# Kernel optimization log

Hardware: AMD Instinct MI355X
Metric: run time of the kernel (lower is better)

## Reference

```python
import jax, jax.numpy as jnp
import numpy as np

B = 2048; IN_DIM = 60; TTL = 30; H = 512; L = 5; OUT = 23
T_PTS = 90; SUB = 10  # fixed-step RK4 substeps per day (stands in for per-sample dopri5)
P_D = 0.2; P_H = 0.15; P_V = 0.25  # DELPHI fixed detection/hospitalization/ventilation fractions
LN2 = float(np.log(2.0))
R_I = LN2/5.0; R_D = LN2/2.0; R_RI = LN2/10.0; R_RH = LN2/15.0; R_RV = LN2/10.0


def setup_inputs():
    ks = jax.random.split(jax.random.key(0), 24)
    w = lambda k, s: (jax.random.normal(k, s) * 0.05).astype(jnp.float32)
    rng = jnp.array([1.0]*11 + [1.0, 60.0, 4.0, 0.5, 0.3, 0.5, 5.0, 5.0, 2.0, 60.0, 30.0, 1.0], dtype=jnp.float32)
    return {
        'model_input': jax.random.normal(ks[0], (B, IN_DIM), dtype=jnp.float32),
        'population': jax.random.uniform(ks[1], (B,), minval=1e5, maxval=1e7, dtype=jnp.float32),
        'cumulative_case_number': jax.random.uniform(ks[2], (B, 1), minval=1e3, maxval=1e5, dtype=jnp.float32),
        'mortality_rate': jax.random.uniform(ks[3], (B,), minval=0.01, maxval=0.05, dtype=jnp.float32),
        'h0': jax.random.normal(ks[4], (L, B, H), dtype=jnp.float32),
        'c0': jax.random.normal(ks[5], (L, B, H), dtype=jnp.float32),
        'W_ih0': w(ks[6], (4*H, TTL)),
        'W_ihR': w(ks[7], (L-1, 4*H, H)),
        'W_hh': w(ks[8], (L, 4*H, H)),
        'b_ih': w(ks[9], (L, 4*H)),
        'b_hh': w(ks[10], (L, 4*H)),
        'meta_W1': w(ks[11], (H, IN_DIM - TTL)), 'meta_b1': w(ks[12], (H,)),
        'meta_W2': w(ks[13], (H, H)), 'meta_b2': w(ks[14], (H,)),
        'ro_W1': w(ks[15], (2*H, 2*H)), 'ro_b1': w(ks[16], (2*H,)),
        'ro_W2': w(ks[17], (OUT, 2*H)), 'ro_b2': w(ks[18], (OUT,)),
        'dnn_output_range': rng,
        'sigmoid_scale': 1,
    }


def _backbone(model_input, population, h0, c0, W_ih0, W_ihR, W_hh, b_ih, b_hh,
              meta_W1, meta_b1, meta_W2, meta_b2, ro_W1, ro_b1, ro_W2, ro_b2,
              dnn_output_range, sigmoid_scale):
    x = model_input[:, :TTL] / population[:, None]
    for l in range(L):  # single-timestep, 5-layer LSTM; torch gate order i,f,g,o
        Wi = W_ih0 if l == 0 else W_ihR[l-1]
        g = x @ Wi.T + b_ih[l] + h0[l] @ W_hh[l].T + b_hh[l]
        gi, gf, gg, go = jnp.split(g, 4, axis=1)
        c = jax.nn.sigmoid(gf) * c0[l] + jax.nn.sigmoid(gi) * jnp.tanh(gg)
        x = jax.nn.sigmoid(go) * jnp.tanh(c)
    ts_out = x  # [B, H]
    m = jax.nn.relu(model_input[:, TTL:] @ meta_W1.T + meta_b1)
    m = jax.nn.relu(m @ meta_W2.T + meta_b2)
    z = jnp.concatenate([ts_out, m], axis=1)  # [B, 2H]
    z = jnp.tanh(z @ ro_W1.T + ro_b1)
    raw = z @ ro_W2.T + ro_b2  # [B, OUT]
    dnn = jax.nn.sigmoid(raw * sigmoid_scale) * dnn_output_range
    return dnn, ts_out, raw


def _ode(dnn, population, cumulative_case_number, mortality_rate):
    p = dnn[:, 11:]  # 12 fitted DELPHI params per sample
    alpha, days, r_s, r_dth, p_dth, r_dthdecay, k1, k2, jump, t_jump, std_normal, k3 = [p[:, j] for j in range(12)]
    N = population
    PopI = cumulative_case_number[:, 0]
    PopD = jnp.floor(mortality_rate * PopI)
    R_0 = jnp.where(PopI - PopD > 5.0 * PopD, 5.0 * PopD, 0.0)
    PopCI = PopI - PopD - R_0
    # DELPHI initial conditions
    S0 = N - (PopCI/P_D)*(k1 + k2) - R_0/P_D - PopD/P_D
    y0 = jnp.stack([
        S0,
        PopCI/P_D*k1,                      # E
        PopCI/P_D*k2,                      # I
        (PopCI/P_D - PopCI)*(1.0 - p_dth), # AR
        PopCI*P_H*(1.0 - p_dth),           # DHR
        PopCI*(1.0 - P_H)*(1.0 - p_dth),   # DQR
        (PopCI/P_D - PopCI)*p_dth,         # AD
        PopCI*P_H*p_dth,                   # DHD
        PopCI*(1.0 - P_H)*p_dth,           # DQD
        R_0/P_D,                           # R
        PopD/P_D,                          # D
        PopCI*P_H,                         # TH
        PopCI*P_H*P_V*(1.0 - p_dth),       # DVR
        PopCI*P_H*P_V*p_dth,               # DVD
        PopD,                              # DD
        PopI,                              # DT
    ], axis=1)  # [B, 16]

    def deriv(t, y):
        S, E, I = y[:, 0], y[:, 1], y[:, 2]
        AR, DHR, DQR, AD, DHD, DQD = y[:, 3], y[:, 4], y[:, 5], y[:, 6], y[:, 7], y[:, 8]
        DVR, DVD = y[:, 12], y[:, 13]
        gam = (2.0/jnp.pi)*jnp.arctan(-(t - days)/20.0*r_s) + 1.0 \
              + jump*jnp.exp(-(t - t_jump)**2/(2.0*std_normal**2))
        pdt = (2.0/jnp.pi)*(p_dth - 0.001)*(jnp.arctan(-t*r_dthdecay/20.0) + jnp.pi/2.0) + 0.001
        inf = alpha*gam*S*I/N
        det = R_D*I
        return jnp.stack([
            -inf,
            inf - R_I*E,
            R_I*E - det,
            det*(1.0-pdt)*(1.0-P_D) - R_RI*AR,
            det*(1.0-pdt)*P_D*P_H - R_RH*DHR,
            det*(1.0-pdt)*P_D*(1.0-P_H) - R_RI*DQR,
            det*pdt*(1.0-P_D) - r_dth*AD,
            det*pdt*P_D*P_H - r_dth*DHD,
            det*pdt*P_D*(1.0-P_H) - r_dth*DQD,
            R_RI*(AR + DQR) + R_RH*DHR,
            r_dth*(AD + DQD + DHD),
            det*P_D*P_H,
            det*(1.0-pdt)*P_D*P_H*P_V - R_RV*DVR,
            det*pdt*P_D*P_H*P_V - r_dth*DVD,
            r_dth*(DHD + DQD),
            det*P_D,
        ], axis=1)

    dt = 1.0 / SUB

    def segment(y, t0):
        def sub(yy, j):
            t = t0 + j*dt
            k1_ = deriv(t, yy)
            k2_ = deriv(t + 0.5*dt, yy + 0.5*dt*k1_)
            k3_ = deriv(t + 0.5*dt, yy + 0.5*dt*k2_)
            k4_ = deriv(t + dt, yy + dt*k3_)
            return yy + (dt/6.0)*(k1_ + 2.0*k2_ + 2.0*k3_ + k4_), None
        y2, _ = jax.lax.scan(sub, y, jnp.arange(SUB, dtype=jnp.float32))
        return y2, y2

    _, ys = jax.lax.scan(segment, y0, jnp.arange(T_PTS - 1, dtype=jnp.float32))
    sol = jnp.concatenate([y0[None], ys], axis=0)  # [T_PTS, B, 16]
    return jnp.transpose(sol, (1, 0, 2))  # [B, T_PTS, 16]


def reference(model_input, population, cumulative_case_number, mortality_rate, h0, c0,
              W_ih0, W_ihR, W_hh, b_ih, b_hh, meta_W1, meta_b1, meta_W2, meta_b2,
              ro_W1, ro_b1, ro_W2, ro_b2, dnn_output_range, sigmoid_scale):
    dnn, ts_out, raw = _backbone(model_input, population, h0, c0, W_ih0, W_ihR, W_hh,
                                 b_ih, b_hh, meta_W1, meta_b1, meta_W2, meta_b2,
                                 ro_W1, ro_b1, ro_W2, ro_b2, dnn_output_range, sigmoid_scale)
    sol = _ode(dnn, population, cumulative_case_number, mortality_rate)
    return sol, dnn, ts_out[:, None, :], raw
```

## Files before the change

kernel.cpp:

```cpp
#include <hip/hip_runtime.h>
#include <hip/hip_bf16.h>
#include <math.h>

#define BATCH 2048
#define HID 512
#define TPTS 90
#define NSEG 89
#define NSUB 10
#define NSTEPS 890

#if defined(__has_builtin)
#if __has_builtin(__builtin_amdgcn_global_load_lds)
#define HAS_GLL 1
#endif
#endif
#ifndef HAS_GLL
#define HAS_GLL 0
#endif

__device__ __constant__ const float kR_I  = 0.6931471805599453f / 5.0f;
__device__ __constant__ const float kR_D  = 0.6931471805599453f / 2.0f;
__device__ __constant__ const float kR_RI = 0.6931471805599453f / 10.0f;
__device__ __constant__ const float kR_RH = 0.6931471805599453f / 15.0f;
__device__ __constant__ const float kR_RV = 0.6931471805599453f / 10.0f;

typedef __attribute__((ext_vector_type(8))) short short8;
typedef __attribute__((ext_vector_type(4))) short short4v;
typedef __attribute__((ext_vector_type(4))) float float4v;

__device__ __forceinline__ float sigmoidf_(float x) { return 1.0f / (1.0f + expf(-x)); }

#if HAS_GLL
__device__ __forceinline__ void gll16(const void* g, void* l) {
    __builtin_amdgcn_global_load_lds(
        (const __attribute__((address_space(1))) unsigned int*)g,
        (__attribute__((address_space(3))) unsigned int*)l, 16, 0, 0);
}
#endif

__global__ void prep_pad(const float* __restrict__ mi, const float* __restrict__ pop,
                         const float* __restrict__ Wih0, const float* __restrict__ mW1,
                         float* __restrict__ x0p, float* __restrict__ xmp,
                         float* __restrict__ Wp0, float* __restrict__ Wpm)
{
    int i = blockIdx.x * 256 + threadIdx.x;
    int r = i >> 5, c = i & 31;
    bool v = (c < 30);
    x0p[i] = v ? mi[r * 60 + c] / pop[r] : 0.0f;
    xmp[i] = v ? mi[r * 60 + 30 + c] : 0.0f;
    Wp0[i] = v ? Wih0[r * 30 + c] : 0.0f;
    if (r < 512) Wpm[i] = v ? mW1[r * 30 + c] : 0.0f;
}

__device__ __forceinline__ void pack_quad(const float* __restrict__ s1, int ld1, int K1,
                                          const float* __restrict__ s2, int ld2, int K2,
                                          __hip_bfloat16* __restrict__ dst, int idx, bool wm)
{
    int Ks = K1 + K2, Kq = Ks >> 2;
    int r = idx / Kq, k4 = (idx - r * Kq) << 2;
    const float* srcp; int base, seg, kk;
    if (k4 < K1) { srcp = s1 + (size_t)r * ld1 + k4; base = 0; seg = K1; kk = k4; }
    else { kk = k4 - K1; srcp = s2 + (size_t)r * ld2 + kk; base = 3 * K1; seg = K2; }
    float4 x = *(const float4*)srcp;
    union { __hip_bfloat16 b[4]; short4v v; } H, L;
    H.b[0] = __float2bfloat16(x.x); H.b[1] = __float2bfloat16(x.y);
    H.b[2] = __float2bfloat16(x.z); H.b[3] = __float2bfloat16(x.w);
    L.b[0] = __float2bfloat16(x.x - __bfloat162float(H.b[0]));
    L.b[1] = __float2bfloat16(x.y - __bfloat162float(H.b[1]));
    L.b[2] = __float2bfloat16(x.z - __bfloat162float(H.b[2]));
    L.b[3] = __float2bfloat16(x.w - __bfloat162float(H.b[3]));
    __hip_bfloat16* d = dst + (size_t)r * (3 * Ks) + base;
    *(short4v*)(d + kk)           = H.v;
    *(short4v*)(d + seg + kk)     = wm ? L.v : H.v;
    *(short4v*)(d + 2 * seg + kk) = wm ? H.v : L.v;
}

__global__ void pack_pair(const float* __restrict__ a1, int alda1, int aK1,
                          const float* __restrict__ a2, int alda2, int aK2,
                          __hip_bfloat16* __restrict__ da, int arows,
                          const float* __restrict__ w1, int wld1, int wK1,
                          const float* __restrict__ w2, int wld2, int wK2,
                          __hip_bfloat16* __restrict__ dw, int wrows)
{
    int aKq = (aK1 + aK2) >> 2, wKq = (wK1 + wK2) >> 2;
    int qa = arows * aKq;
    int idx = blockIdx.x * 256 + threadIdx.x;
    if (idx < qa) {
        pack_quad(a1, alda1, aK1, a2, alda2, aK2, da, idx, false);
    } else {
        idx -= qa;
        if (idx < wrows * wKq) pack_quad(w1, wld1, wK1, w2, wld2, wK2, dw, idx, true);
    }
}

template<int ACT>
__global__ __launch_bounds__(256, 2)
void gemm_mfma(const __hip_bfloat16* __restrict__ Ah,
               const __hip_bfloat16* __restrict__ Wh, int K3,
               const float* __restrict__ b1, const float* __restrict__ b2,
               float* __restrict__ Cp, int ldc, int N)
{
    __shared__ __hip_bfloat16 As[128 * 32];
    __shared__ __hip_bfloat16 Ws[64 * 32];
    const int tid  = threadIdx.x;
    const int m0   = blockIdx.y * 128;
    const int n0   = blockIdx.x * 64;
    const int lane = tid & 63, wv = tid >> 6;
    const int mw   = (wv >> 1) * 64, nw = (wv & 1) * 32;
    const int l15  = lane & 15, quad = lane >> 4;
    const int sr   = tid >> 2;
    const int sc   = (tid & 3) * 8;

    float4v acc[4][2];
    #pragma unroll
    for (int i = 0; i < 4; ++i)
        #pragma unroll
        for (int j = 0; j < 2; ++j)
            acc[i][j] = (float4v){0.0f, 0.0f, 0.0f, 0.0f};

    const __hip_bfloat16* pa0 = Ah + (size_t)(m0 + sr)      * K3 + sc;
    const __hip_bfloat16* pa1 = Ah + (size_t)(m0 + sr + 64) * K3 + sc;
    const __hip_bfloat16* pw0 = Wh + (size_t)(n0 + sr)      * K3 + sc;

#if HAS_GLL
    char* ldsA0 = (char*)As + wv * 1024;
    char* ldsA1 = (char*)As + 4096 + wv * 1024;
    char* ldsW0 = (char*)Ws + wv * 1024;
#endif

#if !HAS_GLL
    short8 a0 = *(const short8*)(pa0);
    short8 a1 = *(const short8*)(pa1);
    short8 w0 = *(const short8*)(pw0);
#endif

    for (int kt = 0; kt < K3; kt += 32) {
#if HAS_GLL
        __syncthreads();
        gll16(pa0 + kt, ldsA0);
        gll16(pa1 + kt, ldsA1);
        gll16(pw0 + kt, ldsW0);
        __syncthreads();
#else
        __syncthreads();
        *(short8*)(As + sr * 32 + sc)        = a0;
        *(short8*)(As + (sr + 64) * 32 + sc) = a1;
        *(short8*)(Ws + sr * 32 + sc)        = w0;
        __syncthreads();
        int kn = kt + 32;
        if (kn < K3) {
            a0 = *(const short8*)(pa0 + kn);
            a1 = *(const short8*)(pa1 + kn);
            w0 = *(const short8*)(pw0 + kn);
        }
#endif
        short8 af[4], bf[2];
        #pragma unroll
        for (int t = 0; t < 4; ++t)
            af[t] = *(const short8*)(As + (mw + t * 16 + l15) * 32 + quad * 8);
        #pragma unroll
        for (int t = 0; t < 2; ++t)
            bf[t] = *(const short8*)(Ws + (nw + t * 16 + l15) * 32 + quad * 8);
        #pragma unroll
        for (int i = 0; i < 4; ++i)
            #pragma unroll
            for (int j = 0; j < 2; ++j)
                acc[i][j] = __builtin_amdgcn_mfma_f32_16x16x32_bf16(af[i], bf[j], acc[i][j], 0, 0, 0);
    }

    #pragma unroll
    for (int j = 0; j < 2; ++j) {
        int col = n0 + nw + j * 16 + l15;
        float bias = b1[col] + (b2 ? b2[col] : 0.0f);
        #pragma unroll
        for (int i = 0; i < 4; ++i) {
            #pragma unroll
            for (int r = 0; r < 4; ++r) {
                int row = m0 + mw + i * 16 + quad * 4 + r;
                float v = acc[i][j][r] + bias;
                if (ACT == 1)      v = fmaxf(v, 0.0f);
                else if (ACT == 2) v = tanhf(v);
                Cp[(size_t)row * ldc + col] = v;
            }
        }
    }
}

template<int ACT>
__global__ __launch_bounds__(256)
void gemm_dual(const float* __restrict__ A1, int lda1,
               const float* __restrict__ W1, int ldw1, int K1,
               const float* __restrict__ A2, int lda2,
               const float* __restrict__ W2, int ldw2, int K2,
               const float* __restrict__ b1p, const float* __restrict__ b2p,
               float* __restrict__ Cp, int ldc, int N)
{
    __shared__ float As[8][128];
    __shared__ float Ws[8][128];
    const int tid  = threadIdx.x;
    const int m0   = blockIdx.y * 128;
    const int n0   = blockIdx.x * 128;
    const int tm   = tid >> 4;
    const int tn   = tid & 15;
    const int lrow = tid >> 1;
    const int lkh  = (tid & 1) << 2;
    const int wrow = n0 + lrow;
    const int Ktot = K1 + K2;

    float acc[8][8];
    #pragma unroll
    for (int i = 0; i < 8; ++i)
        #pragma unroll
        for (int j = 0; j < 8; ++j) acc[i][j] = 0.0f;

    float4 av = *(const float4*)(A1 + (size_t)(m0 + lrow) * lda1 + lkh);
    float4 wv = make_float4(0.0f, 0.0f, 0.0f, 0.0f);
    if (wrow < N) wv = *(const float4*)(W1 + (size_t)wrow * ldw1 + lkh);

    for (int kt = 0; kt < Ktot; kt += 8) {
        __syncthreads();
        As[lkh + 0][lrow] = av.x; As[lkh + 1][lrow] = av.y;
        As[lkh + 2][lrow] = av.z; As[lkh + 3][lrow] = av.w;
        Ws[lkh + 0][lrow] = wv.x; Ws[lkh + 1][lrow] = wv.y;
        Ws[lkh + 2][lrow] = wv.z; Ws[lkh + 3][lrow] = wv.w;
        __syncthreads();

        int kn = kt + 8;
        float4 avn = make_float4(0.0f, 0.0f, 0.0f, 0.0f);
        float4 wvn = avn;
        if (kn < Ktot) {
            if (kn < K1) {
                avn = *(const float4*)(A1 + (size_t)(m0 + lrow) * lda1 + kn + lkh);
                if (wrow < N) wvn = *(const float4*)(W1 + (size_t)wrow * ldw1 + kn + lkh);
            } else {
                int k2 = kn - K1;
                avn = *(const float4*)(A2 + (size_t)(m0 + lrow) * lda2 + k2 + lkh);
                if (wrow < N) wvn = *(const float4*)(W2 + (size_t)wrow * ldw2 + k2 + lkh);
            }
        }

        #pragma unroll
        for (int kk = 0; kk < 8; ++kk) {
            float af[8], wf[8];
            #pragma unroll
            for (int i = 0; i < 4; ++i) {
                af[i]     = As[kk][tm * 8 + i];
                af[i + 4] = As[kk][tm * 8 + 4 + i];
                wf[i]     = Ws[kk][tn * 4 + i];
                wf[i + 4] = Ws[kk][64 + tn * 4 + i];
            }
            #pragma unroll
            for (int i = 0; i < 8; ++i)
                #pragma unroll
                for (int j = 0; j < 8; ++j)
                    acc[i][j] += af[i] * wf[j];
        }
        av = avn; wv = wvn;
    }

    #pragma unroll
    for (int j = 0; j < 8; ++j) {
        int col = n0 + ((j < 4) ? (tn * 4 + j) : (64 + tn * 4 + (j - 4)));
        if (col >= N) continue;
        float bias = b1p[col] + (b2p ? b2p[col] : 0.0f);
        #pragma unroll
        for (int i = 0; i < 8; ++i) {
            int rrow = m0 + tm * 8 + i;
            float v = acc[i][j] + bias;
            if (ACT == 1) v = fmaxf(v, 0.0f);
            else if (ACT == 2) v = tanhf(v);
            Cp[(size_t)rrow * ldc + col] = v;
        }
    }
}

__global__ __launch_bounds__(256)
void gemv_ro2(const float* __restrict__ A, const float* __restrict__ W,
              const float* __restrict__ b, const int* __restrict__ ssp,
              const float* __restrict__ rng, float* __restrict__ raw,
              float* __restrict__ dnn)
{
    int m    = blockIdx.x * 4 + (threadIdx.x >> 6);
    int lane = threadIdx.x & 63;
    const float* ar = A + (size_t)m * 1024 + lane * 4;
    float4 a0 = *(const float4*)(ar);
    float4 a1 = *(const float4*)(ar + 256);
    float4 a2 = *(const float4*)(ar + 512);
    float4 a3 = *(const float4*)(ar + 768);
    int v = *ssp;
    float ss = (v > 100000 || v < 0) ? __int_as_float(v) : (float)v;
    #pragma unroll 1
    for (int n = 0; n < 23; ++n) {
        const float* wr = W + (size_t)n * 1024 + lane * 4;
        float4 w0 = *(const float4*)(wr);
        float4 w1 = *(const float4*)(wr + 256);
        float4 w2 = *(const float4*)(wr + 512);
        float4 w3 = *(const float4*)(wr + 768);
        float s = a0.x * w0.x + a0.y * w0.y + a0.z * w0.z + a0.w * w0.w
                + a1.x * w1.x + a1.y * w1.y + a1.z * w1.z + a1.w * w1.w
                + a2.x * w2.x + a2.y * w2.y + a2.z * w2.z + a2.w * w2.w
                + a3.x * w3.x + a3.y * w3.y + a3.z * w3.z + a3.w * w3.w;
        #pragma unroll
        for (int o = 32; o > 0; o >>= 1) s += __shfl_xor(s, o, 64);
        if (lane == 0) {
            float r2 = s + b[n];
            raw[m * 23 + n] = r2;
            dnn[m * 23 + n] = sigmoidf_(r2 * ss) * rng[n];
        }
    }
}

__global__ void lstm_gates(const float* __restrict__ G_, const float* __restrict__ c0l,
                           float* __restrict__ xout, int xld, float* __restrict__ ts)
{
    int i = blockIdx.x * 256 + threadIdx.x;
    int m = i >> 9, h = i & 511;
    const float* g = G_ + (size_t)m * 2048 + h;
    float gi = g[0], gf = g[512], gg = g[1024], go = g[1536];
    float c = sigmoidf_(gf) * c0l[i] + sigmoidf_(gi) * tanhf(gg);
    float x = sigmoidf_(go) * tanhf(c);
    xout[(size_t)m * xld + h] = x;
    if (ts) ts[i] = x;
}

__global__ void dnn_kernel(const float* __restrict__ raw, const int* __restrict__ ssp,
                           const float* __restrict__ rng, float* __restrict__ dnn)
{
    int i = blockIdx.x * 256 + threadIdx.x;
    if (i >= 2048 * 23) return;
    int c = i % 23;
    int v = *ssp;
    float ss = (v > 100000 || v < 0) ? __int_as_float(v) : (float)v;
    dnn[i] = sigmoidf_(raw[i] * ss) * rng[c];
}

__device__ __forceinline__ void gampdt_eval(float t, float alpha, float days, float rs20,
                                            float jump, float t_jump, float inv2s2,
                                            float pconst, float rdd20, float* ag, float* pd)
{
    float dtj = t - t_jump;
    float g = 0.6366197723675814f * atanf((days - t) * rs20) + 1.0f + jump * expf(-(dtj * dtj) * inv2s2);
    *ag = alpha * g;
    *pd = pconst * (atanf(-t * rdd20) + 1.5707963267948966f) + 0.001f;
}

__global__ void gampdt4_kernel(const float* __restrict__ dnn, const float* __restrict__ pop,
                               float4* __restrict__ ag4)
{
    int idx = blockIdx.x * 256 + threadIdx.x;
    if (idx >= NSTEPS * 2048) return;
    int e = idx & 2047;
    int k = idx >> 11;
    int s = k / 10, j = k - s * 10;
    const float* p = dnn + e * 23 + 11;
    float alpha = p[0], days = p[1], r_s = p[2], p_dth = p[4], r_dthdecay = p[5];
    float jump = p[8], t_jump = p[9], stdn = p[10];
    float invN = 1.0f / pop[e];
    float rs20   = r_s * 0.05f;
    float rdd20  = r_dthdecay * 0.05f;
    float inv2s2 = 1.0f / (2.0f * stdn * stdn);
    float pconst = 0.6366197723675814f * (p_dth - 0.001f);
    float t = (float)s + (float)j * 0.1f;
    float agh, pdh, ag1, pd1;
    gampdt_eval(t + 0.05f, alpha, days, rs20, jump, t_jump, inv2s2, pconst, rdd20, &agh, &pdh);
    gampdt_eval(t + 0.1f,  alpha, days, rs20, jump, t_jump, inv2s2, pconst, rdd20, &ag1, &pd1);
    ag4[idx] = make_float4(agh * invN, pdh, ag1 * invN, pd1);
}

__global__ __launch_bounds__(64)
void ode_core(const float* __restrict__ dnn, const float* __restrict__ pop,
              const float* __restrict__ ccn, const float* __restrict__ mort,
              const float4* __restrict__ ag4, float4* __restrict__ det4,
              float* __restrict__ sol)
{
    int e = blockIdx.x * 64 + threadIdx.x;
    const float* p = dnn + e * 23 + 11;
    float alpha = p[0], days = p[1], r_s = p[2], k1p = p[6], k2p = p[7];
    float jump = p[8], t_jump = p[9], stdn = p[10], p_dth = p[4], rdd = p[5];

    float N = pop[e];
    float invN = 1.0f / N;
    float PopI = ccn[e];
    float PopD = floorf(mort[e] * PopI);
    float R0v  = (PopI - PopD > 5.0f * PopD) ? 5.0f * PopD : 0.0f;
    float PopCI = PopI - PopD - R0v;
    float DP = PopCI / 0.2f;

    float y0 = N - DP * (k1p + k2p) - R0v / 0.2f - PopD / 0.2f;
    float y1 = DP * k1p;
    float y2 = DP * k2p;
    float y11 = PopCI * 0.15f;
    float y15 = PopI;

    float* sole = sol + (size_t)e * (TPTS * 16);
    sole[0] = y0; sole[1] = y1; sole[2] = y2; sole[11] = y11; sole[15] = y15;

    float rs20   = r_s * 0.05f;
    float rdd20  = rdd * 0.05f;
    float inv2s2 = 1.0f / (2.0f * stdn * stdn);
    float pconst = 0.6366197723675814f * (p_dth - 0.001f);
    float ag0, pd0;
    gampdt_eval(0.0f, alpha, days, rs20, jump, t_jump, inv2s2, pconst, rdd20, &ag0, &pd0);
    float agI = ag0 * invN;

    float4 cv[10];
    #pragma unroll
    for (int j = 0; j < 10; ++j) cv[j] = ag4[(size_t)j * 2048 + e];

    const float h6 = 0.016666668f;
    for (int s = 0; s < NSEG; ++s) {
        float Sdet = 0.0f;
        #pragma unroll
        for (int j = 0; j < 10; ++j) {
            float agh = cv[j].x, ag1 = cv[j].z;
            int kn = (s + 1) * 10 + j;
            if (kn >= NSTEPS) kn = NSTEPS - 1;
            cv[j] = ag4[(size_t)kn * 2048 + e];

            float det1 = kR_D * y2;
            float t1   = kR_I * y1;
            float inf  = agI * y0 * y2;
            float d1 = inf - t1, d2 = t1 - det1;
            float a0 = -inf, a1 = d1, a2 = d2;
            float z0 = y0 - 0.05f * inf, z1 = y1 + 0.05f * d1, z2 = y2 + 0.05f * d2;
            float det2 = kR_D * z2; t1 = kR_I * z1; inf = agh * z0 * z2;
            d1 = inf - t1; d2 = t1 - det2;
            a0 -= 2.0f * inf; a1 += 2.0f * d1; a2 += 2.0f * d2;
            z0 = y0 - 0.05f * inf; z1 = y1 + 0.05f * d1; z2 = y2 + 0.05f * d2;
            float det3 = kR_D * z2; t1 = kR_I * z1; inf = agh * z0 * z2;
            d1 = inf - t1; d2 = t1 - det3;
            a0 -= 2.0f * inf; a1 += 2.0f * d1; a2 += 2.0f * d2;
            z0 = y0 - 0.1f * inf; z1 = y1 + 0.1f * d1; z2 = y2 + 0.1f * d2;
            float det4v = kR_D * z2; t1 = kR_I * z1; inf = ag1 * z0 * z2;
            d1 = inf - t1; d2 = t1 - det4v;
            a0 -= inf; a1 += d1; a2 += d2;

            y0 += h6 * a0; y1 += h6 * a1; y2 += h6 * a2;
            float Wd = det1;
            Wd += 2.0f * det2; Wd += 2.0f * det3; Wd += det4v;
            Sdet += Wd;
            det4[(size_t)(s * 10 + j) * 2048 + e] = make_float4(det1, det2, det3, det4v);
            agI = ag1;
        }
        y11 += h6 * (0.03f * Sdet);
        y15 += h6 * (0.2f * Sdet);
        float* sp = sole + (size_t)(s + 1) * 16;
        sp[0] = y0; sp[1] = y1; sp[2] = y2; sp[11] = y11; sp[15] = y15;
    }
}

__global__ __launch_bounds__(64)
void ode_decay(const float* __restrict__ dnn, const float* __restrict__ ccn,
               const float* __restrict__ mort, const float4* __restrict__ ag4,
               const float4* __restrict__ det4, float* __restrict__ sol)
{
    const int t  = blockIdx.x * 64 + threadIdx.x;
    const int e  = t >> 3;
    const int g  = t & 7;
    const int lane = threadIdx.x & 63;
    const int base = lane & ~7;

    const float* p = dnn + e * 23 + 11;
    float r_dth = p[3], p_dth = p[4];

    float PopI = ccn[e];
    float PopD = floorf(mort[e] * PopI);
    float R0v  = (PopI - PopD > 5.0f * PopD) ? 5.0f * PopD : 0.0f;
    float PopCI = PopI - PopD - R0v;
    float DP = PopCI / 0.2f;
    float ompd = 1.0f - p_dth;

    float iy3  = (DP - PopCI) * ompd;
    float iy4  = PopCI * 0.15f * ompd;
    float iy5  = PopCI * 0.85f * ompd;
    float iy6  = (DP - PopCI) * p_dth;
    float iy7  = PopCI * 0.15f * p_dth;
    float iy8  = PopCI * 0.85f * p_dth;
    float iy12 = PopCI * 0.15f * 0.25f * ompd;
    float iy13 = PopCI * 0.15f * 0.25f * p_dth;

    float ha = (g == 0) ? iy3 : (g == 1) ? iy4 : (g == 2) ? iy5 : iy6;
    float hb = (g == 4) ? iy7 : (g == 5) ? iy8 : (g == 6) ? iy12 : iy13;
    float ys = (g < 4) ? ha : hb;
    float c1 = (g == 0) ? 0.8f : (g == 1) ? 0.03f : (g == 2) ? 0.17f : (g == 6) ? 0.0075f : 0.0f;
    float c2 = (g == 3) ? 0.8f : (g == 4) ? 0.03f : (g == 5) ? 0.17f : (g == 7) ? 0.0075f : 0.0f;
    float rr = (g == 0 || g == 2) ? kR_RI : (g == 1) ? kR_RH : (g == 6) ? kR_RV : r_dth;
    int own_idx = (g < 4) ? ((g < 2) ? (g == 0 ? 3 : 4) : (g == 2 ? 5 : 6))
                          : ((g < 6) ? (g == 4 ? 7 : 8) : (g == 6 ? 12 : 13));

    float y9  = R0v / 0.2f;
    float y10 = PopD / 0.2f;
    float y14 = PopD;

    float* sole = sol + (size_t)e * (TPTS * 16);
    sole[own_idx] = ys;
    if (g == 0) sole[9]  = y9;
    if (g == 1) sole[10] = y10;
    if (g == 2) sole[14] = y14;

    float pconst = 0.6366197723675814f * (p_dth - 0.001f);
    float pd0 = pconst * 1.5707963267948966f + 0.001f;
    float u0 = c1 * (1.0f - pd0) + c2 * pd0;

    float4 cvd[10], cva[10];
    #pragma unroll
    for (int j = 0; j < 10; ++j) {
        cvd[j] = det4[(size_t)j * 2048 + e];
        cva[j] = ag4[(size_t)j * 2048 + e];
    }

    const float h6 = 0.016666668f;
    for (int s = 0; s < NSEG; ++s) {
        float Sy = 0.0f;
        #pragma unroll
        for (int j = 0; j < 10; ++j) {
            float4 dd = cvd[j];
            float pdh = cva[j].y, pd1 = cva[j].w;
            int kn = (s + 1) * 10 + j;
            if (kn >= NSTEPS) kn = NSTEPS - 1;
            cvd[j] = det4[(size_t)kn * 2048 + e];
            cva[j] = ag4[(size_t)kn * 2048 + e];

            float uh = c1 * (1.0f - pdh) + c2 * pdh;
            float u1 = c1 * (1.0f - pd1) + c2 * pd1;
            float k1v = dd.x * u0 - rr * ys;
            float zs1 = ys + 0.05f * k1v;
            float k2v = dd.y * uh - rr * zs1;
            float zs2 = ys + 0.05f * k2v;
            float k3v = dd.z * uh - rr * zs2;
            float zs3 = ys + 0.1f * k3v;
            float k4v = dd.w * u1 - rr * zs3;
            float ka = k1v + 2.0f * (k2v + k3v) + k4v;
            Sy += ys + 2.0f * (zs1 + zs2) + zs3;
            ys += h6 * ka;
            u0 = u1;
        }
        float S0 = __shfl(Sy, base + 0, 64);
        float S1 = __shfl(Sy, base + 1, 64);
        float S2 = __shfl(Sy, base + 2, 64);
        float S3 = __shfl(Sy, base + 3, 64);
        float S4 = __shfl(Sy, base + 4, 64);
        float S5 = __shfl(Sy, base + 5, 64);
        y9  += h6 * (kR_RI * (S0 + S2) + kR_RH * S1);
        y10 += h6 * (r_dth * ((S3 + S4) + S5));
        y14 += h6 * (r_dth * (S4 + S5));

        float* sp = sole + (size_t)(s + 1) * 16;
        sp[own_idx] = ys;
        if (g == 0) sp[9]  = y9;
        if (g == 1) sp[10] = y10;
        if (g == 2) sp[14] = y14;
    }
}

__device__ __forceinline__ void deriv16(const float* y, float ag, float pd,
                                        float invN, float r_dth, float* d)
{
    float inf = ag * y[0] * y[2] * invN;
    float det = kR_D * y[2];
    float t1  = kR_I * y[1];
    float omp = 1.0f - pd;
    float dq  = det * omp;
    float dp  = det * pd;
    float dq003 = dq * 0.03f;
    float dp003 = dp * 0.03f;
    d[0]  = -inf;
    d[1]  = inf - t1;
    d[2]  = t1 - det;
    d[3]  = dq * 0.8f  - kR_RI * y[3];
    d[4]  = dq003      - kR_RH * y[4];
    d[5]  = dq * 0.17f - kR_RI * y[5];
    d[6]  = dp * 0.8f  - r_dth * y[6];
    d[7]  = dp003      - r_dth * y[7];
    d[8]  = dp * 0.17f - r_dth * y[8];
    d[9]  = kR_RI * (y[3] + y[5]) + kR_RH * y[4];
    d[10] = r_dth * ((y[6] + y[7]) + y[8]);
    d[11] = det * 0.03f;
    d[12] = 0.25f * dq003 - kR_RV * y[12];
    d[13] = 0.25f * dp003 - r_dth * y[13];
    d[14] = r_dth * (y[7] + y[8]);
    d[15] = det * 0.2f;
}

__global__ __launch_bounds__(64)
void ode_kernel(const float* __restrict__ dnn, const float* __restrict__ pop,
                const float* __restrict__ ccn, const float* __restrict__ mort,
                float* __restrict__ sol)
{
    int e = blockIdx.x * 64 + threadIdx.x;
    const float* p = dnn + e * 23 + 11;
    float alpha = p[0], days = p[1], r_s = p[2], r_dth = p[3], p_dth = p[4];
    float r_dthdecay = p[5], k1p = p[6], k2p = p[7], jump = p[8], t_jump = p[9], stdn = p[10];

    float N = pop[e];
    float invN = 1.0f / N;
    float PopI = ccn[e];
    float PopD = floorf(mort[e] * PopI);
    float R0v  = (PopI - PopD > 5.0f * PopD) ? 5.0f * PopD : 0.0f;
    float PopCI = PopI - PopD - R0v;
    float DP = PopCI / 0.2f;

    float y[16];
    y[0]  = N - DP * (k1p + k2p) - R0v / 0.2f - PopD / 0.2f;
    y[1]  = DP * k1p;
    y[2]  = DP * k2p;
    y[3]  = (DP - PopCI) * (1.0f - p_dth);
    y[4]  = PopCI * 0.15f * (1.0f - p_dth);
    y[5]  = PopCI * 0.85f * (1.0f - p_dth);
    y[6]  = (DP - PopCI) * p_dth;
    y[7]  = PopCI * 0.15f * p_dth;
    y[8]  = PopCI * 0.85f * p_dth;
    y[9]  = R0v / 0.2f;
    y[10] = PopD / 0.2f;
    y[11] = PopCI * 0.15f;
    y[12] = PopCI * 0.15f * 0.25f * (1.0f - p_dth);
    y[13] = PopCI * 0.15f * 0.25f * p_dth;
    y[14] = PopD;
    y[15] = PopI;

    {
        float* sp = sol + (size_t)e * (TPTS * 16);
        #pragma unroll
        for (int i = 0; i < 16; ++i) sp[i] = y[i];
    }

    float rs20   = r_s * 0.05f;
    float rdd20  = r_dthdecay * 0.05f;
    float inv2s2 = 1.0f / (2.0f * stdn * stdn);
    float pconst = 0.6366197723675814f * (p_dth - 0.001f);

    float ag0, pd0;
    gampdt_eval(0.0f, alpha, days, rs20, jump, t_jump, inv2s2, pconst, rdd20, &ag0, &pd0);

    for (int s = 0; s < NSEG; ++s) {
        float t0 = (float)s;
        for (int j = 0; j < NSUB; ++j) {
            float agh, pdh, ag1, pd1;
            float t = t0 + (float)j * 0.1f;
            gampdt_eval(t + 0.05f, alpha, days, rs20, jump, t_jump, inv2s2, pconst, rdd20, &agh, &pdh);
            gampdt_eval(t + 0.1f,  alpha, days, rs20, jump, t_jump, inv2s2, pconst, rdd20, &ag1, &pd1);
            float d[16], acc[16], yt[16];
            deriv16(y, ag0, pd0, invN, r_dth, d);
            #pragma unroll
            for (int i = 0; i < 16; ++i) { acc[i] = d[i]; yt[i] = y[i] + 0.05f * d[i]; }
            deriv16(yt, agh, pdh, invN, r_dth, d);
            #pragma unroll
            for (int i = 0; i < 16; ++i) { acc[i] += 2.0f * d[i]; yt[i] = y[i] + 0.05f * d[i]; }
            deriv16(yt, agh, pdh, invN, r_dth, d);
            #pragma unroll
            for (int i = 0; i < 16; ++i) { acc[i] += 2.0f * d[i]; yt[i] = y[i] + 0.1f * d[i]; }
            deriv16(yt, ag1, pd1, invN, r_dth, d);
            #pragma unroll
            for (int i = 0; i < 16; ++i) y[i] += 0.016666668f * (acc[i] + d[i]);
            ag0 = ag1; pd0 = pd1;
        }
        float* sp = sol + (size_t)e * (TPTS * 16) + (size_t)(s + 1) * 16;
        #pragma unroll
        for (int i = 0; i < 16; ++i) sp[i] = y[i];
    }
}

extern "C" void kernel_launch(void* const* d_in, const int* in_sizes, int n_in,
                              void* d_out, int out_size, void* d_ws, size_t ws_size,
                              hipStream_t stream)
{
    const float* mi   = (const float*)d_in[0];
    const float* pop  = (const float*)d_in[1];
    const float* ccn  = (const float*)d_in[2];
    const float* mort = (const float*)d_in[3];
    const float* h0   = (const float*)d_in[4];
    const float* c0   = (const float*)d_in[5];
    const float* Wih0 = (const float*)d_in[6];
    const float* WihR = (const float*)d_in[7];
    const float* Whh  = (const float*)d_in[8];
    const float* bih  = (const float*)d_in[9];
    const float* bhh  = (const float*)d_in[10];
    const float* mW1  = (const float*)d_in[11];
    const float* mb1  = (const float*)d_in[12];
    const float* mW2  = (const float*)d_in[13];
    const float* mb2  = (const float*)d_in[14];
    const float* rW1  = (const float*)d_in[15];
    const float* rb1  = (const float*)d_in[16];
    const float* rW2  = (const float*)d_in[17];
    const float* rb2  = (const float*)d_in[18];
    const float* rng  = (const float*)d_in[19];
    const int*   ssp  = (const int*)d_in[20];

    float* out   = (float*)d_out;
    float* sol_o = out;
    float* dnn_o = out + 2949120;
    float* ts_o  = out + 2949120 + 47104;
    float* raw_o = out + 2949120 + 47104 + 1048576;

    float* ws  = (float*)d_ws;
    float* G   = ws;
    float* Z   = ws + 4194304;
    float* X0  = ws + 6291456;
    float* X1  = ws + 7340032;
    float* x0p = ws + 8388608;
    float* xmp = ws + 8454144;
    float* Wp0 = ws + 8519680;
    float* Wpm = ws + 8585216;
    __hip_bfloat16* Ab = (__hip_bfloat16*)(ws + 8601600);
    __hip_bfloat16* Wb = (__hip_bfloat16*)(ws + 8601600 + 3145728);
    float4* AG4  = (float4*)(ws + 8601600);
    float4* DET4 = (float4*)ws;
    bool wsOK = ws_size >= (size_t)15892480 * sizeof(float);

    prep_pad<<<256, 256, 0, stream>>>(mi, pop, Wih0, mW1, x0p, xmp, Wp0, Wpm);

    gemm_dual<1><<<dim3(4, 16), 256, 0, stream>>>(xmp, 32, Wpm, 32, 32,
                                                  nullptr, 0, nullptr, 0, 0,
                                                  mb1, nullptr, G, 512, 512);

    if (wsOK) {
        pack_pair<<<(2048 * 128 + 512 * 128 + 255) / 256, 256, 0, stream>>>(
            G, 512, 512, nullptr, 0, 0, Ab, 2048,
            mW2, 512, 512, nullptr, 0, 0, Wb, 512);
        gemm_mfma<1><<<dim3(8, 16), 256, 0, stream>>>(Ab, Wb, 1536, mb2, nullptr, Z + 512, 1024, 512);

        for (int l = 0; l < 5; ++l) {
            const float* A1 = (l == 0) ? x0p : ((l & 1) ? X1 : X0);
            int          K1 = (l == 0) ? 32 : 512;
            const float* W1 = (l == 0) ? Wp0 : (WihR + (size_t)(l - 1) * 1048576);
            int Ks = K1 + 512, K3 = 3 * Ks, Kq = Ks >> 2;
            pack_pair<<<(2048 * Kq * 2 + 255) / 256, 256, 0, stream>>>(
                A1, K1, K1, h0 + (size_t)l * 1048576, 512, 512, Ab, 2048,
                W1, K1, K1, Whh + (size_t)l * 1048576, 512, 512, Wb, 2048);
            gemm_mfma<0><<<dim3(32, 16), 256, 0, stream>>>(
                Ab, Wb, K3, bih + l * 2048, bhh + l * 2048, G, 2048, 2048);
            float* xo  = (l == 4) ? Z : ((l & 1) ? X0 : X1);
            int    xol = (l == 4) ? 1024 : 512;
            lstm_gates<<<4096, 256, 0, stream>>>(G, c0 + (size_t)l * 1048576, xo, xol,
                                                 (l == 4) ? ts_o : nullptr);
        }

        pack_pair<<<(2048 * 256 + 1024 * 256 + 255) / 256, 256, 0, stream>>>(
            Z, 1024, 1024, nullptr, 0, 0, Ab, 2048,
            rW1, 1024, 1024, nullptr, 0, 0, Wb, 1024);
        gemm_mfma<2><<<dim3(16, 16), 256, 0, stream>>>(Ab, Wb, 3072, rb1, nullptr, G, 1024, 1024);

        gemv_ro2<<<512, 256, 0, stream>>>(G, rW2, rb2, ssp, rng, raw_o, dnn_o);

        gampdt4_kernel<<<(NSTEPS * 2048 + 255) / 256, 256, 0, stream>>>(dnn_o, pop, AG4);
        ode_core<<<32, 64, 0, stream>>>(dnn_o, pop, ccn, mort, AG4, DET4, sol_o);
        ode_decay<<<256, 64, 0, stream>>>(dnn_o, ccn, mort, AG4, DET4, sol_o);
    } else {
        gemm_dual<1><<<dim3(4, 16), 256, 0, stream>>>(G, 512, mW2, 512, 512,
                                                      nullptr, 0, nullptr, 0, 0,
                                                      mb2, nullptr, Z + 512, 1024, 512);
        for (int l = 0; l < 5; ++l) {
            const float* A1 = (l == 0) ? x0p : ((l & 1) ? X1 : X0);
            int          K1 = (l == 0) ? 32 : 512;
            const float* W1 = (l == 0) ? Wp0 : (WihR + (size_t)(l - 1) * 1048576);
            gemm_dual<0><<<dim3(16, 16), 256, 0, stream>>>(
                A1, K1, W1, K1, K1,
                h0 + (size_t)l * 1048576, 512, Whh + (size_t)l * 1048576, 512, 512,
                bih + l * 2048, bhh + l * 2048, G, 2048, 2048);
            float* xo  = (l == 4) ? Z : ((l & 1) ? X0 : X1);
            int    xol = (l == 4) ? 1024 : 512;
            lstm_gates<<<4096, 256, 0, stream>>>(G, c0 + (size_t)l * 1048576, xo, xol,
                                                 (l == 4) ? ts_o : nullptr);
        }
        gemm_dual<2><<<dim3(8, 16), 256, 0, stream>>>(Z, 1024, rW1, 1024, 1024,
                                                      nullptr, 0, nullptr, 0, 0,
                                                      rb1, nullptr, G, 1024, 1024);
        gemm_dual<0><<<dim3(1, 16), 256, 0, stream>>>(G, 1024, rW2, 1024, 1024,
                                                      nullptr, 0, nullptr, 0, 0,
                                                      rb2, nullptr, raw_o, 23, 23);
        dnn_kernel<<<184, 256, 0, stream>>>(raw_o, ssp, rng, dnn_o);
        ode_kernel<<<32, 64, 0, stream>>>(dnn_o, pop, ccn, mort, sol_o);
    }
    (void)in_sizes; (void)n_in; (void)out_size;
}
```

Measured before the change: 794.7 us.

## Widen MFMA GEMM tile to 128x128, add split-K for LSTM gates, drop global_load_lds

The bf16 MFMA GEMM now computes a 128x128 tile per block (4x4 MFMA accumulators per wave) instead of 128x64, which raises reuse of each loaded A and W fragment. The LSTM gate GEMMs get a two-way split-K along blockIdx.z when the workspace is large enough, writing partial sums to a second buffer that lstm_gates adds back in. This restores the grid size lost to the wider tile. The global_load_lds path is removed in favour of register-staged prefetch. The costs are higher register pressure from the larger accumulator set, an extra 16 MB partial-sum write and read per layer, and a dependency on extra workspace.

```diff
diff --git a/kernel.cpp b/kernel.cpp
--- a/kernel.cpp
+++ b/kernel.cpp
@@ -9,15 +9,6 @@
 #define NSUB 10
 #define NSTEPS 890
 
-#if defined(__has_builtin)
-#if __has_builtin(__builtin_amdgcn_global_load_lds)
-#define HAS_GLL 1
-#endif
-#endif
-#ifndef HAS_GLL
-#define HAS_GLL 0
-#endif
-
 __device__ __constant__ const float kR_I  = 0.6931471805599453f / 5.0f;
 __device__ __constant__ const float kR_D  = 0.6931471805599453f / 2.0f;
 __device__ __constant__ const float kR_RI = 0.6931471805599453f / 10.0f;
@@ -29,14 +20,6 @@
 typedef __attribute__((ext_vector_type(4))) float float4v;
 
 __device__ __forceinline__ float sigmoidf_(float x) { return 1.0f / (1.0f + expf(-x)); }
-
-#if HAS_GLL
-__device__ __forceinline__ void gll16(const void* g, void* l) {
-    __builtin_amdgcn_global_load_lds(
-        (const __attribute__((address_space(1))) unsigned int*)g,
-        (__attribute__((address_space(3))) unsigned int*)l, 16, 0, 0);
-}
-#endif
 
 __global__ void prep_pad(const float* __restrict__ mi, const float* __restrict__ pop,
                          const float* __restrict__ Wih0, const float* __restrict__ mW1,
@@ -96,82 +79,75 @@
 template<int ACT>
 __global__ __launch_bounds__(256, 2)
 void gemm_mfma(const __hip_bfloat16* __restrict__ Ah,
-               const __hip_bfloat16* __restrict__ Wh, int K3,
+               const __hip_bfloat16* __restrict__ Wh, int K3, int kHalf,
                const float* __restrict__ b1, const float* __restrict__ b2,
-               float* __restrict__ Cp, int ldc, int N)
+               float* __restrict__ Cp, float* __restrict__ Cp2, int ldc, int N)
 {
     __shared__ __hip_bfloat16 As[128 * 32];
-    __shared__ __hip_bfloat16 Ws[64 * 32];
+    __shared__ __hip_bfloat16 Ws[128 * 32];
     const int tid  = threadIdx.x;
     const int m0   = blockIdx.y * 128;
-    const int n0   = blockIdx.x * 64;
+    const int n0   = blockIdx.x * 128;
+    const int z    = blockIdx.z;
+    const int k0   = z ? kHalf : 0;
+    const int kLen = (kHalf == 0) ? K3 : (z ? (K3 - kHalf) : kHalf);
+    float* C = z ? Cp2 : Cp;
     const int lane = tid & 63, wv = tid >> 6;
-    const int mw   = (wv >> 1) * 64, nw = (wv & 1) * 32;
+    const int mw   = (wv >> 1) * 64, nw = (wv & 1) * 64;
     const int l15  = lane & 15, quad = lane >> 4;
     const int sr   = tid >> 2;
     const int sc   = (tid & 3) * 8;
 
-    float4v acc[4][2];
+    float4v acc[4][4];
     #pragma unroll
     for (int i = 0; i < 4; ++i)
         #pragma unroll
-        for (int j = 0; j < 2; ++j)
+        for (int j = 0; j < 4; ++j)
             acc[i][j] = (float4v){0.0f, 0.0f, 0.0f, 0.0f};
 
-    const __hip_bfloat16* pa0 = Ah + (size_t)(m0 + sr)      * K3 + sc;
-    const __hip_bfloat16* pa1 = Ah + (size_t)(m0 + sr + 64) * K3 + sc;
-    const __hip_bfloat16* pw0 = Wh + (size_t)(n0 + sr)      * K3 + sc;
-
-#if HAS_GLL
-    char* ldsA0 = (char*)As + wv * 1024;
-    char* ldsA1 = (char*)As + 4096 + wv * 1024;
-    char* ldsW0 = (char*)Ws + wv * 1024;
-#endif
-
-#if !HAS_GLL
+    const __hip_bfloat16* pa0 = Ah + (size_t)(m0 + sr)      * K3 + k0 + sc;
+    const __hip_bfloat16* pa1 = Ah + (size_t)(m0 + sr + 64) * K3 + k0 + sc;
+    const __hip_bfloat16* pw0 = Wh + (size_t)(n0 + sr)      * K3 + k0 + sc;
+    const __hip_bfloat16* pw1 = Wh + (size_t)(n0 + sr + 64) * K3 + k0 + sc;
+
     short8 a0 = *(const short8*)(pa0);
     short8 a1 = *(const short8*)(pa1);
     short8 w0 = *(const short8*)(pw0);
-#endif
-
-    for (int kt = 0; kt < K3; kt += 32) {
-#if HAS_GLL
-        __syncthreads();
-        gll16(pa0 + kt, ldsA0);
-        gll16(pa1 + kt, ldsA1);
-        gll16(pw0 + kt, ldsW0);
-        __syncthreads();
-#else
+    short8 w1 = *(const short8*)(pw1);
+
+    for (int kt = 0; kt < kLen; kt += 32) {
         __syncthreads();
         *(short8*)(As + sr * 32 + sc)        = a0;
         *(short8*)(As + (sr + 64) * 32 + sc) = a1;
         *(short8*)(Ws + sr * 32 + sc)        = w0;
+        *(short8*)(Ws + (sr + 64) * 32 + sc) = w1;
         __syncthreads();
+
         int kn = kt + 32;
-        if (kn < K3) {
+        if (kn < kLen) {
             a0 = *(const short8*)(pa0 + kn);
             a1 = *(const short8*)(pa1 + kn);
             w0 = *(const short8*)(pw0 + kn);
-        }
-#endif
-        short8 af[4], bf[2];
-        #pragma unroll
-        for (int t = 0; t < 4; ++t)
+            w1 = *(const short8*)(pw1 + kn);
+        }
+
+        short8 af[4], bf[4];
+        #pragma unroll
+        for (int t = 0; t < 4; ++t) {
             af[t] = *(const short8*)(As + (mw + t * 16 + l15) * 32 + quad * 8);
-        #pragma unroll
-        for (int t = 0; t < 2; ++t)
             bf[t] = *(const short8*)(Ws + (nw + t * 16 + l15) * 32 + quad * 8);
+        }
         #pragma unroll
         for (int i = 0; i < 4; ++i)
             #pragma unroll
-            for (int j = 0; j < 2; ++j)
+            for (int j = 0; j < 4; ++j)
                 acc[i][j] = __builtin_amdgcn_mfma_f32_16x16x32_bf16(af[i], bf[j], acc[i][j], 0, 0, 0);
     }
 
     #pragma unroll
-    for (int j = 0; j < 2; ++j) {
+    for (int j = 0; j < 4; ++j) {
         int col = n0 + nw + j * 16 + l15;
-        float bias = b1[col] + (b2 ? b2[col] : 0.0f);
+        float bias = z ? 0.0f : (b1[col] + (b2 ? b2[col] : 0.0f));
         #pragma unroll
         for (int i = 0; i < 4; ++i) {
             #pragma unroll
@@ -180,7 +156,7 @@
                 float v = acc[i][j][r] + bias;
                 if (ACT == 1)      v = fmaxf(v, 0.0f);
                 else if (ACT == 2) v = tanhf(v);
-                Cp[(size_t)row * ldc + col] = v;
+                C[(size_t)row * ldc + col] = v;
             }
         }
     }
@@ -310,13 +286,18 @@
     }
 }
 
-__global__ void lstm_gates(const float* __restrict__ G_, const float* __restrict__ c0l,
+__global__ void lstm_gates(const float* __restrict__ G0, const float* __restrict__ G1,
+                           const float* __restrict__ c0l,
                            float* __restrict__ xout, int xld, float* __restrict__ ts)
 {
     int i = blockIdx.x * 256 + threadIdx.x;
     int m = i >> 9, h = i & 511;
-    const float* g = G_ + (size_t)m * 2048 + h;
+    const float* g = G0 + (size_t)m * 2048 + h;
     float gi = g[0], gf = g[512], gg = g[1024], go = g[1536];
+    if (G1) {
+        const float* g2 = G1 + (size_t)m * 2048 + h;
+        gi += g2[0]; gf += g2[512]; gg += g2[1024]; go += g2[1536];
+    }
     float c = sigmoidf_(gf) * c0l[i] + sigmoidf_(gi) * tanhf(gg);
     float x = sigmoidf_(go) * tanhf(c);
     xout[(size_t)m * xld + h] = x;
@@ -705,7 +686,9 @@
     __hip_bfloat16* Wb = (__hip_bfloat16*)(ws + 8601600 + 3145728);
     float4* AG4  = (float4*)(ws + 8601600);
     float4* DET4 = (float4*)ws;
-    bool wsOK = ws_size >= (size_t)15892480 * sizeof(float);
+    float*  G1   = ws + 15892480;
+    bool wsOK  = ws_size >= (size_t)15892480 * sizeof(float);
+    bool wsOK2 = ws_size >= (size_t)(15892480 + 4194304) * sizeof(float);
 
     prep_pad<<<256, 256, 0, stream>>>(mi, pop, Wih0, mW1, x0p, xmp, Wp0, Wpm);
 
@@ -717,7 +700,8 @@
         pack_pair<<<(2048 * 128 + 512 * 128 + 255) / 256, 256, 0, stream>>>(
             G, 512, 512, nullptr, 0, 0, Ab, 2048,
             mW2, 512, 512, nullptr, 0, 0, Wb, 512);
-        gemm_mfma<1><<<dim3(8, 16), 256, 0, stream>>>(Ab, Wb, 1536, mb2, nullptr, Z + 512, 1024, 512);
+        gemm_mfma<1><<<dim3(4, 16, 1), 256, 0, stream>>>(Ab, Wb, 1536, 0, mb2, nullptr,
+                                                         Z + 512, nullptr, 1024, 512);
 
         for (int l = 0; l < 5; ++l) {
             const float* A1 = (l == 0) ? x0p : ((l & 1) ? X1 : X0);
@@ -727,18 +711,21 @@
             pack_pair<<<(2048 * Kq * 2 + 255) / 256, 256, 0, stream>>>(
                 A1, K1, K1, h0 + (size_t)l * 1048576, 512, 512, Ab, 2048,
                 W1, K1, K1, Whh + (size_t)l * 1048576, 512, 512, Wb, 2048);
-            gemm_mfma<0><<<dim3(32, 16), 256, 0, stream>>>(
-                Ab, Wb, K3, bih + l * 2048, bhh + l * 2048, G, 2048, 2048);
+            int kh = wsOK2 ? (((K3 / 2) + 31) / 32) * 32 : 0;
+            gemm_mfma<0><<<dim3(16, 16, wsOK2 ? 2 : 1), 256, 0, stream>>>(
+                Ab, Wb, K3, kh, bih + l * 2048, bhh + l * 2048, G, G1, 2048, 2048);
             float* xo  = (l == 4) ? Z : ((l & 1) ? X0 : X1);
             int    xol = (l == 4) ? 1024 : 512;
-            lstm_gates<<<4096, 256, 0, stream>>>(G, c0 + (size_t)l * 1048576, xo, xol,
+            lstm_gates<<<4096, 256, 0, stream>>>(G, wsOK2 ? G1 : nullptr,
+                                                 c0 + (size_t)l * 1048576, xo, xol,
                                                  (l == 4) ? ts_o : nullptr);
         }
 
         pack_pair<<<(2048 * 256 + 1024 * 256 + 255) / 256, 256, 0, stream>>>(
             Z, 1024, 1024, nullptr, 0, 0, Ab, 2048,
             rW1, 1024, 1024, nullptr, 0, 0, Wb, 1024);
-        gemm_mfma<2><<<dim3(16, 16), 256, 0, stream>>>(Ab, Wb, 3072, rb1, nullptr, G, 1024, 1024);
+        gemm_mfma<2><<<dim3(8, 16, 1), 256, 0, stream>>>(Ab, Wb, 3072, 0, rb1, nullptr,
+                                                         G, nullptr, 1024, 1024);
 
         gemv_ro2<<<512, 256, 0, stream>>>(G, rW2, rb2, ssp, rng, raw_o, dnn_o);
 
@@ -759,7 +746,7 @@
                 bih + l * 2048, bhh + l * 2048, G, 2048, 2048);
             float* xo  = (l == 4) ? Z : ((l & 1) ? X0 : X1);
             int    xol = (l == 4) ? 1024 : 512;
-            lstm_gates<<<4096, 256, 0, stream>>>(G, c0 + (size_t)l * 1048576, xo, xol,
+            lstm_gates<<<4096, 256, 0, stream>>>(G, nullptr, c0 + (size_t)l * 1048576, xo, xol,
                                                  (l == 4) ? ts_o : nullptr);
         }
         gemm_dual<2><<<dim3(8, 16), 256, 0, stream>>>(Z, 1024, rW1, 1024, 1024,
```

New measurement: 748.7 us. 5.8% less time.
